# Kernel tuning notes

Hardware: AMD Instinct MI355X
Metric: run time of the kernel (lower is better)

The kernel has to match this reference:

```python
import jax, jax.numpy as jnp
import numpy as np
from jax.ops import segment_sum, segment_max

N, E, G = 50000, 800000, 64   # nodes, edges, graphs
H, C = 3, 64                   # heads, out channels per head
IN, ED = 75, 1                 # in feature dim, edge feature dim


def gat_conv(x, edge_index, edge_attr, W, a_src, a_dst, We, a_e, bias):
    """PyG GATConv (concat heads, self-loops with fill_value='mean', eval mode)."""
    n = x.shape[0]
    xh = (x @ W).reshape(n, H, C)                       # [n,H,C]
    src, dst = edge_index[0], edge_index[1]
    # self-loop edge_attr = mean of incoming edge_attr per node
    ones = jnp.ones((src.shape[0],), x.dtype)
    cnt = segment_sum(ones, dst, num_segments=n)
    loop_attr = segment_sum(edge_attr, dst, num_segments=n) / jnp.maximum(cnt, 1.0)[:, None]
    loops = jnp.arange(n)
    s = jnp.concatenate([src, loops])
    d = jnp.concatenate([dst, loops])
    ea = jnp.concatenate([edge_attr, loop_attr], axis=0)
    eh = (ea @ We).reshape(-1, H, C)                    # [E+n,H,C]
    asrc = (xh * a_src).sum(-1)                         # [n,H]
    adst = (xh * a_dst).sum(-1)
    alpha = asrc[s] + adst[d] + (eh * a_e).sum(-1)      # [E+n,H]
    alpha = jax.nn.leaky_relu(alpha, 0.2)
    # segment softmax over destination nodes
    amax = segment_max(alpha, d, num_segments=n)
    ex = jnp.exp(alpha - amax[d])
    denom = segment_sum(ex, d, num_segments=n)
    attn = ex / (denom[d] + 1e-16)                      # [E+n,H]
    out = segment_sum(xh[s] * attn[:, :, None], d, num_segments=n)
    return out.reshape(n, H * C) + bias, attn


def setup_inputs() -> dict:
    key = jax.random.key(0)
    ks = jax.random.split(key, 24)
    f = lambda k, sh, sc: (jax.random.normal(k, sh, jnp.float32) * sc)
    inp = {
        "x": f(ks[0], (N, IN), 1.0),
        "edge_attr": jax.random.uniform(ks[1], (E, ED), jnp.float32),
        "W1": f(ks[2], (IN, H * C), 0.1),
        "att_src1": f(ks[3], (H, C), 0.1),
        "att_dst1": f(ks[4], (H, C), 0.1),
        "We1": f(ks[5], (ED, H * C), 0.1),
        "att_e1": f(ks[6], (H, C), 0.1),
        "b1": f(ks[7], (H * C,), 0.1),
        "W2": f(ks[8], (H * C, H * C), 0.1),
        "att_src2": f(ks[9], (H, C), 0.1),
        "att_dst2": f(ks[10], (H, C), 0.1),
        "We2": f(ks[11], (ED, H * C), 0.1),
        "att_e2": f(ks[12], (H, C), 0.1),
        "b2": f(ks[13], (H * C,), 0.1),
        "fc1_w": f(ks[14], (H * C * 2, C), 0.1),
        "fc1_b": f(ks[15], (C,), 0.1),
        "fc2_w": f(ks[16], (C, 1), 0.1),
        "fc2_b": f(ks[17], (1,), 0.1),
        "edge_index": jax.random.randint(ks[18], (2, E), 0, N, jnp.int64),
        "batch": jnp.sort(jax.random.randint(ks[19], (N,), 0, G, jnp.int64)),
    }
    return inp


def reference(x, edge_attr, W1, att_src1, att_dst1, We1, att_e1, b1,
              W2, att_src2, att_dst2, We2, att_e2, b2,
              fc1_w, fc1_b, fc2_w, fc2_b, edge_index, batch):
    h, attn1 = gat_conv(x, edge_index, edge_attr, W1, att_src1, att_dst1, We1, att_e1, b1)
    h = jax.nn.elu(h)
    h, attn2 = gat_conv(h, edge_index, edge_attr, W2, att_src2, att_dst2, We2, att_e2, b2)
    h = jax.nn.elu(h)
    # global mean / max pooling over graphs
    cnt = segment_sum(jnp.ones((N,), h.dtype), batch, num_segments=G)
    x_mean = segment_sum(h, batch, num_segments=G) / jnp.maximum(cnt, 1.0)[:, None]
    x_max = segment_max(h, batch, num_segments=G)
    z = jnp.concatenate([x_mean, x_max], axis=1)        # [G, 2*H*C]
    z = jax.nn.relu(z @ fc1_w + fc1_b)
    logits = (z @ fc2_w + fc2_b)[:, 0]                  # [G]
    return logits, attn1, attn2
```

## Files before the change

kernel.cpp:

```cpp
#include <hip/hip_runtime.h>
#include <hip/hip_bf16.h>

typedef unsigned int u32;
typedef __attribute__((ext_vector_type(8))) short short8;
typedef __attribute__((ext_vector_type(4))) float f32x4;

#define NN 50000
#define NPAD 50048
#define EE 800000
#define GG 64
#define HH 3
#define CC 64
#define IN_DIM 75
#define KP1 96
#define HC 192
#define TOTAL (EE + NN)

__device__ __forceinline__ u32 fmap(float f) {
    u32 u = __float_as_uint(f);
    return (u & 0x80000000u) ? ~u : (u | 0x80000000u);
}
__device__ __forceinline__ float funmap(u32 m) {
    u32 u = (m & 0x80000000u) ? (m ^ 0x80000000u) : ~m;
    return __uint_as_float(u);
}

__global__ void k_deg(const int* __restrict__ ei, const float* __restrict__ eattr,
                      int* __restrict__ deg, float* __restrict__ attrsum) {
    int e = blockIdx.x * 256 + threadIdx.x;
    if (e >= EE) return;
    int d = ei[EE + e];
    atomicAdd(&deg[d], 1);
    atomicAdd(&attrsum[d], eattr[e]);
}

__global__ void k_scan1(const int* __restrict__ deg, u32* __restrict__ startv,
                        u32* __restrict__ blocksum) {
    __shared__ u32 sh[1024];
    int t = threadIdx.x;
    int n = blockIdx.x * 1024 + t;
    u32 v = (n < NN) ? (u32)(deg[n] + 1) : 0u;
    u32 val = v;
    sh[t] = val;
    __syncthreads();
    for (int off = 1; off < 1024; off <<= 1) {
        u32 y = (t >= off) ? sh[t - off] : 0u;
        __syncthreads();
        val += y;
        sh[t] = val;
        __syncthreads();
    }
    if (n < NN) startv[n] = val - v;
    if (t == 0) blocksum[blockIdx.x] = sh[1023];
}

__global__ void k_scan2(u32* __restrict__ blocksum, int nb) {
    if (threadIdx.x == 0) {
        u32 acc = 0;
        for (int b = 0; b < nb; b++) { u32 t = blocksum[b]; blocksum[b] = acc; acc += t; }
    }
}

__global__ void k_scan3(u32* __restrict__ startv, const u32* __restrict__ blocksum,
                        u32* __restrict__ cursor) {
    int n = blockIdx.x * 256 + threadIdx.x;
    if (n >= NN) return;
    u32 s = startv[n] + blocksum[n >> 10];
    startv[n] = s;
    cursor[n] = s;
}

__global__ void k_gcnt(const int* __restrict__ batch, int* __restrict__ pcnt) {
    int g = threadIdx.x;
    if (g >= GG) return;
    int lo0 = 0, hi0 = NN;
    while (lo0 < hi0) { int mid = (lo0 + hi0) >> 1; if (batch[mid] < g) lo0 = mid + 1; else hi0 = mid; }
    int lo1 = lo0, hi1 = NN;
    while (lo1 < hi1) { int mid = (lo1 + hi1) >> 1; if (batch[mid] < g + 1) lo1 = mid + 1; else hi1 = mid; }
    pcnt[g] = lo1 - lo0;
}

__global__ void k_fill(const int* __restrict__ ei, const float* __restrict__ eattr,
                       const float* __restrict__ attrsum, const int* __restrict__ deg,
                       u32* __restrict__ cursor, int* __restrict__ srcP,
                       int* __restrict__ dstP, float* __restrict__ eaP,
                       u32* __restrict__ iOf) {
    int i = blockIdx.x * 256 + threadIdx.x;
    if (i >= TOTAL) return;
    int s, d;
    float ea;
    if (i < EE) {
        s = ei[i]; d = ei[EE + i]; ea = eattr[i];
    } else {
        s = d = i - EE;
        ea = attrsum[s] / fmaxf((float)deg[s], 1.f);
    }
    u32 pos = atomicAdd(&cursor[d], 1u);
    srcP[pos] = s;
    dstP[pos] = d;
    eaP[pos] = ea;
    iOf[pos] = (u32)i;
}

__global__ void k_prep(const float* __restrict__ W1, const float* __restrict__ W2,
                       const float* __restrict__ We1, const float* __restrict__ ae1,
                       const float* __restrict__ We2, const float* __restrict__ ae2,
                       __hip_bfloat16* __restrict__ Wt1, __hip_bfloat16* __restrict__ Wt2,
                       u32* __restrict__ pmax, float* __restrict__ wedot) {
    int i = blockIdx.x * 256 + threadIdx.x;
    if (i < HC * KP1) {
        int j = i / KP1, k = i - j * KP1;
        Wt1[i] = __float2bfloat16(k < IN_DIM ? W1[k * HC + j] : 0.f);
    }
    if (i < HC * HC) {
        int j = i / HC, k = i - j * HC;
        Wt2[i] = __float2bfloat16(W2[k * HC + j]);
    }
    if (i < GG * HC) pmax[i] = 0x007FFFFFu;
    if (blockIdx.x == 0) {
        int w = threadIdx.x >> 6, c = threadIdx.x & 63;
        for (int dd = w; dd < 6; dd += 4) {
            int layer = dd / 3, h = dd - 3 * layer;
            const float* We = layer ? We2 : We1;
            const float* ae = layer ? ae2 : ae1;
            float v = We[h * 64 + c] * ae[h * 64 + c];
#pragma unroll
            for (int off = 32; off; off >>= 1) v += __shfl_xor(v, off, 64);
            if (c == 0) wedot[dd] = v;
        }
    }
}

__global__ void k_xconv(const float* __restrict__ x, __hip_bfloat16* __restrict__ xb) {
    int i = blockIdx.x * 256 + threadIdx.x;
    if (i >= NPAD * KP1) return;
    int n = i / KP1, k = i - n * KP1;
    float v = (n < NN && k < IN_DIM) ? x[n * IN_DIM + k] : 0.f;
    xb[i] = __float2bfloat16(v);
}

template <int KPAD>
__global__ __launch_bounds__(256) void k_mfma_gemm(const __hip_bfloat16* __restrict__ A,
                                                   const __hip_bfloat16* __restrict__ Wt,
                                                   const float* __restrict__ asrcw,
                                                   const float* __restrict__ adstw,
                                                   __hip_bfloat16* __restrict__ outb,
                                                   float* __restrict__ asrc,
                                                   float* __restrict__ adst) {
    int wid = threadIdx.x >> 6;
    int lane = threadIdx.x & 63;
    int r0 = blockIdx.x * 64 + wid * 16;
    int lr = lane & 15;
    int g = lane >> 4;
    const short* Ab = (const short*)A;
    const short* Wb = (const short*)Wt;
    f32x4 acc[12];
#pragma unroll
    for (int f = 0; f < 12; f++) acc[f] = (f32x4){0.f, 0.f, 0.f, 0.f};
#pragma unroll
    for (int k0 = 0; k0 < KPAD; k0 += 32) {
        short8 a = *(const short8*)(Ab + (size_t)(r0 + lr) * KPAD + k0 + 8 * g);
#pragma unroll
        for (int f = 0; f < 12; f++) {
            short8 b = *(const short8*)(Wb + (size_t)(f * 16 + lr) * KPAD + k0 + 8 * g);
            acc[f] = __builtin_amdgcn_mfma_f32_16x16x32_bf16(a, b, acc[f], 0, 0, 0);
        }
    }
    int rbase = r0 + 4 * g;
#pragma unroll
    for (int f = 0; f < 12; f++) {
        int col = f * 16 + lr;
#pragma unroll
        for (int r = 0; r < 4; r++) {
            int row = rbase + r;
            if (row < NN) outb[(size_t)row * HC + col] = __float2bfloat16(acc[f][r]);
        }
    }
    float asw[12], adw[12];
#pragma unroll
    for (int f = 0; f < 12; f++) {
        asw[f] = asrcw[f * 16 + lr];
        adw[f] = adstw[f * 16 + lr];
    }
#pragma unroll
    for (int h = 0; h < 3; h++) {
#pragma unroll
        for (int r = 0; r < 4; r++) {
            float p = acc[4 * h][r] * asw[4 * h] + acc[4 * h + 1][r] * asw[4 * h + 1] +
                      acc[4 * h + 2][r] * asw[4 * h + 2] + acc[4 * h + 3][r] * asw[4 * h + 3];
            float q = acc[4 * h][r] * adw[4 * h] + acc[4 * h + 1][r] * adw[4 * h + 1] +
                      acc[4 * h + 2][r] * adw[4 * h + 2] + acc[4 * h + 3][r] * adw[4 * h + 3];
#pragma unroll
            for (int off = 1; off < 16; off <<= 1) {
                p += __shfl_xor(p, off, 64);
                q += __shfl_xor(q, off, 64);
            }
            int row = rbase + r;
            if (lr == 0 && row < NN) {
                asrc[row * 3 + h] = p;
                adst[row * 3 + h] = q;
            }
        }
    }
}

__global__ void k_alphaP(const int* __restrict__ srcP, const int* __restrict__ dstP,
                         const float* __restrict__ eaP, const float* __restrict__ asrc,
                         const float* __restrict__ adst, const float* __restrict__ wedot,
                         int woff, float* __restrict__ eP) {
    int p = blockIdx.x * 256 + threadIdx.x;
    if (p >= TOTAL) return;
    int s = srcP[p], d = dstP[p];
    float ea = eaP[p];
#pragma unroll
    for (int h = 0; h < 3; h++) {
        float a = asrc[s * 3 + h] + adst[d * 3 + h] + ea * wedot[woff + h];
        a = (a > 0.f) ? a : 0.2f * a;
        eP[(size_t)p * 3 + h] = __expf(a);
    }
}

template <int LAYER2>
__global__ void k_gatherSM(const u32* __restrict__ startv, const int* __restrict__ deg,
                           const int* __restrict__ srcP, const float* __restrict__ eP,
                           const __hip_bfloat16* __restrict__ xhb,
                           const float* __restrict__ bias, float* __restrict__ rdenom,
                           __hip_bfloat16* __restrict__ hb, const int* __restrict__ batch,
                           float* __restrict__ psum, u32* __restrict__ pmax) {
    int n = blockIdx.x;
    int j = threadIdx.x;
    int h = j >> 6, c = j & 63;
    u32 st = startv[n];
    int L = deg[n] + 1;
    const int* sp = srcP + st;
    const float* ep = eP + (size_t)st * 3 + h;

    float acc = 0.f, ssum = 0.f;
    int p = 0;
    for (; p + 8 <= L; p += 8) {
        int s0 = sp[p], s1 = sp[p + 1], s2 = sp[p + 2], s3 = sp[p + 3];
        int s4 = sp[p + 4], s5 = sp[p + 5], s6 = sp[p + 6], s7 = sp[p + 7];
        float e0 = ep[3 * p], e1 = ep[3 * p + 3], e2 = ep[3 * p + 6], e3 = ep[3 * p + 9];
        float e4 = ep[3 * p + 12], e5 = ep[3 * p + 15], e6 = ep[3 * p + 18], e7 = ep[3 * p + 21];
        float x0 = __bfloat162float(xhb[(size_t)s0 * HC + j]);
        float x1 = __bfloat162float(xhb[(size_t)s1 * HC + j]);
        float x2 = __bfloat162float(xhb[(size_t)s2 * HC + j]);
        float x3 = __bfloat162float(xhb[(size_t)s3 * HC + j]);
        float x4 = __bfloat162float(xhb[(size_t)s4 * HC + j]);
        float x5 = __bfloat162float(xhb[(size_t)s5 * HC + j]);
        float x6 = __bfloat162float(xhb[(size_t)s6 * HC + j]);
        float x7 = __bfloat162float(xhb[(size_t)s7 * HC + j]);
        acc += e0 * x0; acc += e1 * x1; acc += e2 * x2; acc += e3 * x3;
        acc += e4 * x4; acc += e5 * x5; acc += e6 * x6; acc += e7 * x7;
        ssum += ((e0 + e1) + (e2 + e3)) + ((e4 + e5) + (e6 + e7));
    }
    for (; p < L; p++) {
        int s0 = sp[p];
        float e0 = ep[3 * p];
        float x0 = __bfloat162float(xhb[(size_t)s0 * HC + j]);
        acc += e0 * x0;
        ssum += e0;
    }
    float r = 1.f / (ssum + 1e-16f);
    if (c == 0) rdenom[n * 3 + h] = r;
    float o = acc * r + bias[j];
    o = (o > 0.f) ? o : expm1f(o);
    if (LAYER2) {
        int gi = batch[n];
        atomicAdd(&psum[gi * HC + j], o);
        atomicMax(&pmax[gi * HC + j], fmap(o));
    } else {
        hb[(size_t)n * HC + j] = __float2bfloat16(o);
    }
}

__global__ void k_attnout(const u32* __restrict__ iOf, const int* __restrict__ dstP,
                          const float* __restrict__ eP, const float* __restrict__ rdenom,
                          float* __restrict__ attn) {
    int pos = blockIdx.x * 256 + threadIdx.x;
    if (pos >= TOTAL) return;
    int d = dstP[pos];
    u32 i = iOf[pos];
    float e0 = eP[(size_t)pos * 3 + 0];
    float e1 = eP[(size_t)pos * 3 + 1];
    float e2 = eP[(size_t)pos * 3 + 2];
    attn[(size_t)i * 3 + 0] = e0 * rdenom[d * 3 + 0];
    attn[(size_t)i * 3 + 1] = e1 * rdenom[d * 3 + 1];
    attn[(size_t)i * 3 + 2] = e2 * rdenom[d * 3 + 2];
}

__global__ void k_head(const float* __restrict__ psum, const u32* __restrict__ pmax,
                       const int* __restrict__ pcnt, const float* __restrict__ fc1w,
                       const float* __restrict__ fc1b, const float* __restrict__ fc2w,
                       const float* __restrict__ fc2b, float* __restrict__ logits) {
    __shared__ float z[2 * HC];
    int g = blockIdx.x;
    int t = threadIdx.x;
    float cnt = fmaxf((float)pcnt[g], 1.f);
    for (int k = t; k < 2 * HC; k += 64)
        z[k] = (k < HC) ? psum[g * HC + k] / cnt : funmap(pmax[g * HC + (k - HC)]);
    __syncthreads();
    float acc = fc1b[t];
    for (int k = 0; k < 2 * HC; k++) acc += z[k] * fc1w[k * 64 + t];
    acc = fmaxf(acc, 0.f);
    float v = acc * fc2w[t];
#pragma unroll
    for (int off = 32; off; off >>= 1) v += __shfl_xor(v, off, 64);
    if (t == 0) logits[g] = v + fc2b[0];
}

extern "C" void kernel_launch(void* const* d_in, const int* in_sizes, int n_in,
                              void* d_out, int out_size, void* d_ws, size_t ws_size,
                              hipStream_t stream) {
    const float* x     = (const float*)d_in[0];
    const float* eattr = (const float*)d_in[1];
    const float* W1    = (const float*)d_in[2];
    const float* as1   = (const float*)d_in[3];
    const float* ad1   = (const float*)d_in[4];
    const float* We1   = (const float*)d_in[5];
    const float* ae1   = (const float*)d_in[6];
    const float* b1    = (const float*)d_in[7];
    const float* W2    = (const float*)d_in[8];
    const float* as2   = (const float*)d_in[9];
    const float* ad2   = (const float*)d_in[10];
    const float* We2   = (const float*)d_in[11];
    const float* ae2   = (const float*)d_in[12];
    const float* b2    = (const float*)d_in[13];
    const float* fc1w  = (const float*)d_in[14];
    const float* fc1b  = (const float*)d_in[15];
    const float* fc2w  = (const float*)d_in[16];
    const float* fc2b  = (const float*)d_in[17];
    const int* ei      = (const int*)d_in[18];
    const int* batch   = (const int*)d_in[19];

    float* logits = (float*)d_out;
    float* attn1  = logits + GG;
    float* attn2  = attn1 + (size_t)TOTAL * 3;

    float* eP      = (float*)d_ws;
    int*   srcP    = (int*)(eP + (size_t)TOTAL * 3);
    int*   dstP    = srcP + TOTAL;
    float* eaP     = (float*)(dstP + TOTAL);
    u32*   iOf     = (u32*)(eaP + TOTAL);
    int*   deg     = (int*)(iOf + TOTAL);
    float* attrsum = (float*)(deg + NN);
    float* asrc    = attrsum + NN;
    float* adst    = asrc + NN * 3;
    float* rdenom  = adst + NN * 3;
    u32*   startv  = (u32*)(rdenom + NN * 3);
    u32*   cursor  = startv + NN;
    u32*   blocksum= cursor + NN;
    float* wedot   = (float*)(blocksum + 64);
    float* psum    = wedot + 8;
    u32*   pmax    = (u32*)(psum + GG * HC);
    int*   pcnt    = (int*)(pmax + GG * HC);
    __hip_bfloat16* xb  = (__hip_bfloat16*)(pcnt + 64);
    __hip_bfloat16* xhb = xb + (size_t)NPAD * KP1;
    __hip_bfloat16* hb  = xhb + (size_t)NPAD * HC;
    __hip_bfloat16* Wt1 = hb + (size_t)NPAD * HC;
    __hip_bfloat16* Wt2 = Wt1 + (size_t)HC * KP1;

    hipMemsetAsync(deg, 0, NN * sizeof(int), stream);
    hipMemsetAsync(attrsum, 0, NN * sizeof(float), stream);
    hipMemsetAsync(psum, 0, GG * HC * sizeof(float), stream);
    hipMemsetAsync(hb + (size_t)NN * HC, 0, (size_t)(NPAD - NN) * HC * sizeof(__hip_bfloat16), stream);

    k_deg<<<(EE + 255) / 256, 256, 0, stream>>>(ei, eattr, deg, attrsum);
    k_scan1<<<49, 1024, 0, stream>>>(deg, startv, blocksum);
    k_scan2<<<1, 64, 0, stream>>>(blocksum, 49);
    k_scan3<<<(NN + 255) / 256, 256, 0, stream>>>(startv, blocksum, cursor);
    k_gcnt<<<1, 64, 0, stream>>>(batch, pcnt);
    k_fill<<<(TOTAL + 255) / 256, 256, 0, stream>>>(ei, eattr, attrsum, deg, cursor,
                                                    srcP, dstP, eaP, iOf);
    k_prep<<<(HC * HC + 255) / 256, 256, 0, stream>>>(W1, W2, We1, ae1, We2, ae2,
                                                      Wt1, Wt2, pmax, wedot);
    k_xconv<<<(NPAD * KP1 + 255) / 256, 256, 0, stream>>>(x, xb);

    const int GB = NPAD / 64;

    k_mfma_gemm<KP1><<<GB, 256, 0, stream>>>(xb, Wt1, as1, ad1, xhb, asrc, adst);
    k_alphaP<<<(TOTAL + 255) / 256, 256, 0, stream>>>(srcP, dstP, eaP, asrc, adst,
                                                      wedot, 0, eP);
    k_gatherSM<0><<<NN, 192, 0, stream>>>(startv, deg, srcP, eP, xhb, b1, rdenom,
                                          hb, batch, psum, pmax);
    k_attnout<<<(TOTAL + 255) / 256, 256, 0, stream>>>(iOf, dstP, eP, rdenom, attn1);

    k_mfma_gemm<HC><<<GB, 256, 0, stream>>>(hb, Wt2, as2, ad2, xhb, asrc, adst);
    k_alphaP<<<(TOTAL + 255) / 256, 256, 0, stream>>>(srcP, dstP, eaP, asrc, adst,
                                                      wedot, 3, eP);
    k_gatherSM<1><<<NN, 192, 0, stream>>>(startv, deg, srcP, eP, xhb, b2, rdenom,
                                          hb, batch, psum, pmax);
    k_attnout<<<(TOTAL + 255) / 256, 256, 0, stream>>>(iOf, dstP, eP, rdenom, attn2);

    k_head<<<GG, 64, 0, stream>>>(psum, pmax, pcnt, fc1w, fc1b, fc2w, fc2b, logits);
}
```

Measured before the change: 652.8 us.

## Pad node features to 256 bf16 and gather with 16-byte vector loads per wave

The GEMM now writes transformed node features with a 256-element row stride and zero-fills the padding. The gather kernel handles one node per wave instead of one per 192-thread block. Each half-wave processes alternate edges, and each lane loads 8 bf16 values with one 16-byte load; the two halves are combined with shuffles at the end. This cuts per-element gather instructions and launch granularity, at the cost of extra memory for padding and about a quarter of the loaded lanes being padding.

```diff
diff --git a/kernel.cpp b/kernel.cpp
--- a/kernel.cpp
+++ b/kernel.cpp
@@ -2,7 +2,9 @@
 #include <hip/hip_bf16.h>
 
 typedef unsigned int u32;
+typedef unsigned short ushort;
 typedef __attribute__((ext_vector_type(8))) short short8;
+typedef __attribute__((ext_vector_type(8))) ushort ushort8;
 typedef __attribute__((ext_vector_type(4))) float f32x4;
 
 #define NN 50000
@@ -14,6 +16,7 @@
 #define IN_DIM 75
 #define KP1 96
 #define HC 192
+#define XS 256
 #define TOTAL (EE + NN)
 
 __device__ __forceinline__ u32 fmap(float f) {
@@ -23,6 +26,9 @@
 __device__ __forceinline__ float funmap(u32 m) {
     u32 u = (m & 0x80000000u) ? (m ^ 0x80000000u) : ~m;
     return __uint_as_float(u);
+}
+__device__ __forceinline__ float bf2f(ushort u) {
+    return __uint_as_float(((u32)u) << 16);
 }
 
 __global__ void k_deg(const int* __restrict__ ei, const float* __restrict__ eattr,
@@ -139,7 +145,7 @@
     xb[i] = __float2bfloat16(v);
 }
 
-template <int KPAD>
+template <int KPAD, int OS>
 __global__ __launch_bounds__(256) void k_mfma_gemm(const __hip_bfloat16* __restrict__ A,
                                                    const __hip_bfloat16* __restrict__ Wt,
                                                    const float* __restrict__ asrcw,
@@ -173,7 +179,16 @@
 #pragma unroll
         for (int r = 0; r < 4; r++) {
             int row = rbase + r;
-            if (row < NN) outb[(size_t)row * HC + col] = __float2bfloat16(acc[f][r]);
+            if (row < NN) outb[(size_t)row * OS + col] = __float2bfloat16(acc[f][r]);
+        }
+    }
+    if (OS > HC) {
+        u32* ob = (u32*)outb;
+        int row0 = blockIdx.x * 64;
+        const int padw = (OS - HC) >> 1;
+        for (int idx = threadIdx.x; idx < 64 * padw; idx += 256) {
+            int row = idx / padw, cc = idx - row * padw;
+            ob[(size_t)(row0 + row) * (OS >> 1) + (HC >> 1) + cc] = 0u;
         }
     }
     float asw[12], adw[12];
@@ -221,56 +236,84 @@
 }
 
 template <int LAYER2>
-__global__ void k_gatherSM(const u32* __restrict__ startv, const int* __restrict__ deg,
-                           const int* __restrict__ srcP, const float* __restrict__ eP,
-                           const __hip_bfloat16* __restrict__ xhb,
+__global__ __launch_bounds__(256) void k_gatherSM(const u32* __restrict__ startv,
+                           const int* __restrict__ deg, const int* __restrict__ srcP,
+                           const float* __restrict__ eP,
+                           const __hip_bfloat16* __restrict__ xhb2,
                            const float* __restrict__ bias, float* __restrict__ rdenom,
                            __hip_bfloat16* __restrict__ hb, const int* __restrict__ batch,
                            float* __restrict__ psum, u32* __restrict__ pmax) {
-    int n = blockIdx.x;
-    int j = threadIdx.x;
-    int h = j >> 6, c = j & 63;
+    int w = threadIdx.x >> 6;
+    int n = blockIdx.x * 4 + w;
+    if (n >= NN) return;
+    int lane = threadIdx.x & 63;
+    int half = lane >> 5;
+    int lc = lane & 31;
+    int myh = lc >> 3; if (myh > 2) myh = 2;
     u32 st = startv[n];
     int L = deg[n] + 1;
     const int* sp = srcP + st;
-    const float* ep = eP + (size_t)st * 3 + h;
-
-    float acc = 0.f, ssum = 0.f;
+    const float* epn = eP + (size_t)st * 3;
+    const ushort* xb = (const ushort*)xhb2;
+
+    float a0=0.f,a1=0.f,a2=0.f,a3=0.f,a4=0.f,a5=0.f,a6=0.f,a7=0.f,ssum=0.f;
+
+#define GSTEP(qv) { int s_ = sp[qv]; float e_ = epn[(size_t)(qv) * 3 + myh];            \
+        ushort8 v_ = *(const ushort8*)(xb + (size_t)s_ * XS + lc * 8);                  \
+        a0 += e_ * bf2f(v_[0]); a1 += e_ * bf2f(v_[1]);                                 \
+        a2 += e_ * bf2f(v_[2]); a3 += e_ * bf2f(v_[3]);                                 \
+        a4 += e_ * bf2f(v_[4]); a5 += e_ * bf2f(v_[5]);                                 \
+        a6 += e_ * bf2f(v_[6]); a7 += e_ * bf2f(v_[7]); ssum += e_; }
+
     int p = 0;
     for (; p + 8 <= L; p += 8) {
-        int s0 = sp[p], s1 = sp[p + 1], s2 = sp[p + 2], s3 = sp[p + 3];
-        int s4 = sp[p + 4], s5 = sp[p + 5], s6 = sp[p + 6], s7 = sp[p + 7];
-        float e0 = ep[3 * p], e1 = ep[3 * p + 3], e2 = ep[3 * p + 6], e3 = ep[3 * p + 9];
-        float e4 = ep[3 * p + 12], e5 = ep[3 * p + 15], e6 = ep[3 * p + 18], e7 = ep[3 * p + 21];
-        float x0 = __bfloat162float(xhb[(size_t)s0 * HC + j]);
-        float x1 = __bfloat162float(xhb[(size_t)s1 * HC + j]);
-        float x2 = __bfloat162float(xhb[(size_t)s2 * HC + j]);
-        float x3 = __bfloat162float(xhb[(size_t)s3 * HC + j]);
-        float x4 = __bfloat162float(xhb[(size_t)s4 * HC + j]);
-        float x5 = __bfloat162float(xhb[(size_t)s5 * HC + j]);
-        float x6 = __bfloat162float(xhb[(size_t)s6 * HC + j]);
-        float x7 = __bfloat162float(xhb[(size_t)s7 * HC + j]);
-        acc += e0 * x0; acc += e1 * x1; acc += e2 * x2; acc += e3 * x3;
-        acc += e4 * x4; acc += e5 * x5; acc += e6 * x6; acc += e7 * x7;
-        ssum += ((e0 + e1) + (e2 + e3)) + ((e4 + e5) + (e6 + e7));
-    }
-    for (; p < L; p++) {
-        int s0 = sp[p];
-        float e0 = ep[3 * p];
-        float x0 = __bfloat162float(xhb[(size_t)s0 * HC + j]);
-        acc += e0 * x0;
-        ssum += e0;
-    }
+        GSTEP(p + half)
+        GSTEP(p + 2 + half)
+        GSTEP(p + 4 + half)
+        GSTEP(p + 6 + half)
+    }
+    for (; p < L; p += 2) {
+        int q = p + half;
+        bool act = q < L;
+        int s_ = act ? sp[q] : 0;
+        float e_ = act ? epn[(size_t)q * 3 + myh] : 0.f;
+        ushort8 v_ = *(const ushort8*)(xb + (size_t)s_ * XS + lc * 8);
+        a0 += e_ * bf2f(v_[0]); a1 += e_ * bf2f(v_[1]);
+        a2 += e_ * bf2f(v_[2]); a3 += e_ * bf2f(v_[3]);
+        a4 += e_ * bf2f(v_[4]); a5 += e_ * bf2f(v_[5]);
+        a6 += e_ * bf2f(v_[6]); a7 += e_ * bf2f(v_[7]); ssum += e_;
+    }
+#undef GSTEP
+
+    a0 += __shfl_xor(a0, 32, 64); a1 += __shfl_xor(a1, 32, 64);
+    a2 += __shfl_xor(a2, 32, 64); a3 += __shfl_xor(a3, 32, 64);
+    a4 += __shfl_xor(a4, 32, 64); a5 += __shfl_xor(a5, 32, 64);
+    a6 += __shfl_xor(a6, 32, 64); a7 += __shfl_xor(a7, 32, 64);
+    ssum += __shfl_xor(ssum, 32, 64);
+
     float r = 1.f / (ssum + 1e-16f);
-    if (c == 0) rdenom[n * 3 + h] = r;
-    float o = acc * r + bias[j];
-    o = (o > 0.f) ? o : expm1f(o);
-    if (LAYER2) {
-        int gi = batch[n];
-        atomicAdd(&psum[gi * HC + j], o);
-        atomicMax(&pmax[gi * HC + j], fmap(o));
-    } else {
-        hb[(size_t)n * HC + j] = __float2bfloat16(o);
+    if (half == 0 && lc < 24) {
+        if ((lc & 7) == 0) rdenom[n * 3 + myh] = r;
+        const f32x4* bp = (const f32x4*)(bias + lc * 8);
+        f32x4 b0 = bp[0], b1 = bp[1];
+        float o[8] = {a0 * r + b0[0], a1 * r + b0[1], a2 * r + b0[2], a3 * r + b0[3],
+                      a4 * r + b1[0], a5 * r + b1[1], a6 * r + b1[2], a7 * r + b1[3]};
+#pragma unroll
+        for (int k = 0; k < 8; k++) o[k] = (o[k] > 0.f) ? o[k] : expm1f(o[k]);
+        if (LAYER2) {
+            int gi = batch[n];
+#pragma unroll
+            for (int k = 0; k < 8; k++) {
+                atomicAdd(&psum[gi * HC + lc * 8 + k], o[k]);
+                atomicMax(&pmax[gi * HC + lc * 8 + k], fmap(o[k]));
+            }
+        } else {
+            short8 hv;
+#pragma unroll
+            for (int k = 0; k < 8; k++)
+                hv[k] = (short)__bfloat16_as_ushort(__float2bfloat16(o[k]));
+            *(short8*)((short*)hb + (size_t)n * HC + lc * 8) = hv;
+        }
     }
 }
 
@@ -354,11 +397,11 @@
     float* psum    = wedot + 8;
     u32*   pmax    = (u32*)(psum + GG * HC);
     int*   pcnt    = (int*)(pmax + GG * HC);
-    __hip_bfloat16* xb  = (__hip_bfloat16*)(pcnt + 64);
-    __hip_bfloat16* xhb = xb + (size_t)NPAD * KP1;
-    __hip_bfloat16* hb  = xhb + (size_t)NPAD * HC;
-    __hip_bfloat16* Wt1 = hb + (size_t)NPAD * HC;
-    __hip_bfloat16* Wt2 = Wt1 + (size_t)HC * KP1;
+    __hip_bfloat16* xb   = (__hip_bfloat16*)(pcnt + 64);
+    __hip_bfloat16* xhb2 = xb + (size_t)NPAD * KP1;
+    __hip_bfloat16* hb   = xhb2 + (size_t)NPAD * XS;
+    __hip_bfloat16* Wt1  = hb + (size_t)NPAD * HC;
+    __hip_bfloat16* Wt2  = Wt1 + (size_t)HC * KP1;
 
     hipMemsetAsync(deg, 0, NN * sizeof(int), stream);
     hipMemsetAsync(attrsum, 0, NN * sizeof(float), stream);
@@ -377,19 +420,20 @@
     k_xconv<<<(NPAD * KP1 + 255) / 256, 256, 0, stream>>>(x, xb);
 
     const int GB = NPAD / 64;
-
-    k_mfma_gemm<KP1><<<GB, 256, 0, stream>>>(xb, Wt1, as1, ad1, xhb, asrc, adst);
+    const int GGB = (NN + 3) / 4;
+
+    k_mfma_gemm<KP1, XS><<<GB, 256, 0, stream>>>(xb, Wt1, as1, ad1, xhb2, asrc, adst);
     k_alphaP<<<(TOTAL + 255) / 256, 256, 0, stream>>>(srcP, dstP, eaP, asrc, adst,
                                                       wedot, 0, eP);
-    k_gatherSM<0><<<NN, 192, 0, stream>>>(startv, deg, srcP, eP, xhb, b1, rdenom,
-                                          hb, batch, psum, pmax);
+    k_gatherSM<0><<<GGB, 256, 0, stream>>>(startv, deg, srcP, eP, xhb2, b1, rdenom,
+                                           hb, batch, psum, pmax);
     k_attnout<<<(TOTAL + 255) / 256, 256, 0, stream>>>(iOf, dstP, eP, rdenom, attn1);
 
-    k_mfma_gemm<HC><<<GB, 256, 0, stream>>>(hb, Wt2, as2, ad2, xhb, asrc, adst);
+    k_mfma_gemm<HC, XS><<<GB, 256, 0, stream>>>(hb, Wt2, as2, ad2, xhb2, asrc, adst);
     k_alphaP<<<(TOTAL + 255) / 256, 256, 0, stream>>>(srcP, dstP, eaP, asrc, adst,
                                                       wedot, 3, eP);
-    k_gatherSM<1><<<NN, 192, 0, stream>>>(startv, deg, srcP, eP, xhb, b2, rdenom,
-                                          hb, batch, psum, pmax);
+    k_gatherSM<1><<<GGB, 256, 0, stream>>>(startv, deg, srcP, eP, xhb2, b2, rdenom,
+                                           hb, batch, psum, pmax);
     k_attnout<<<(TOTAL + 255) / 256, 256, 0, stream>>>(iOf, dstP, eP, rdenom, attn2);
 
     k_head<<<GG, 64, 0, stream>>>(psum, pmax, pcnt, fc1w, fc1b, fc2w, fc2b, logits);
```

Result: slower. 1.450 ms (+122.1%).
